# Performance work log

Hardware: AMD Instinct MI355X
Metric: run time of the kernel (lower is better)

## Reference

```python
import jax, jax.numpy as jnp
import numpy as np
import math

B, S, HID = 16, 1024, 1024
H, D = 16, 64  # heads, head_dim
WINDOW = 512  # pos bias length = 2*WINDOW+1 = 1025


def setup_inputs() -> dict:
    key = jax.random.key(0)
    ks = jax.random.split(key, 12)
    xav = lambda k, shp: jax.random.uniform(k, shp, jnp.float32, -1.0, 1.0) * math.sqrt(6.0 / (shp[0] + shp[1]))
    return {
        "hidden_states": jax.random.normal(ks[0], (B, S, HID), jnp.float32),
        "Wq": xav(ks[1], (HID, HID)), "bq": jnp.zeros((HID,), jnp.float32),
        "Wk": xav(ks[2], (HID, HID)), "bk": jnp.zeros((HID,), jnp.float32),
        "Wv": xav(ks[3], (HID, HID)), "bv": jnp.zeros((HID,), jnp.float32),
        "Wo": xav(ks[4], (HID, HID)), "bo": jnp.zeros((HID,), jnp.float32),
        "W_pe": xav(ks[5], (HID, 1)), "b_pe": jnp.zeros((HID,), jnp.float32),
        "pos_bias": 0.02 * jax.random.normal(ks[6], (1, H, 1, 2 * WINDOW + 1), jnp.float32),
        "clip_info": 0,
    }


def reference(hidden_states, Wq, bq, Wk, bk, Wv, bv, Wo, bo, W_pe, b_pe, pos_bias, clip_info):
    b, s, hid = hidden_states.shape
    mid = s // 2
    # relative positions in [-1, 1), shape [s, 1]
    positions = ((jnp.arange(s) - mid).astype(jnp.float32) / (mid + 1e-6))[:, None]
    pos_emb = positions @ W_pe.T + b_pe  # [s, hid]
    hs = hidden_states + pos_emb

    def heads(x):
        return x.reshape(b, s, H, D).transpose(0, 2, 1, 3)  # [b, H, s, D]

    q = heads(hs @ Wq.T + bq)
    k = heads(hs @ Wk.T + bk)
    v = heads(hs @ Wv.T + bv)

    scores = jnp.einsum("bhqd,bhkd->bhqk", q, k) / math.sqrt(D)
    scores = scores + pos_bias[:, :, :, :s]  # broadcast learned window bias over batch and query
    probs = jax.nn.softmax(scores, axis=-1)  # dropout is identity in eval mode
    ctx = jnp.einsum("bhqk,bhkd->bhqd", probs, v)
    ctx = ctx.transpose(0, 2, 1, 3).reshape(b, s, hid)
    return ctx @ Wo.T + bo
```

## Files before the change

kernel.cpp:

```cpp
#include <hip/hip_runtime.h>
#include <hip/hip_bf16.h>
#include <stdint.h>

#define BATCH 16
#define SEQ   1024
#define HIDN  1024
#define NH    16
#define HD    64
#define PBSTRIDE 1025

#define TS  64
#define AST 76

#define KSCL 0.18033688f
#define L2E  1.44269504f
#define MSUB 11.54156032f

#if __has_builtin(__builtin_amdgcn_exp2f)
#define EXP2(x) __builtin_amdgcn_exp2f(x)
#else
#define EXP2(x) exp2f(x)
#endif

typedef __attribute__((ext_vector_type(8))) short short8;
typedef __attribute__((ext_vector_type(4))) short short4v;
typedef __attribute__((ext_vector_type(4))) float f32x4;

__device__ __forceinline__ float bf2f(short x) {
    unsigned int u = ((unsigned int)(unsigned short)x) << 16;
    union { unsigned int u; float f; } c; c.u = u; return c.f;
}
__device__ __forceinline__ short f2bf(float f) {
    union { float f; unsigned int u; } c; c.f = f;
    unsigned int r = c.u + 0x7FFFu + ((c.u >> 16) & 1u);
    return (short)(r >> 16);
}
__device__ __forceinline__ short f2bf_fast(float f) {
    __hip_bfloat16 h = __float2bfloat16(f);
    return *reinterpret_cast<short*>(&h);
}

typedef __attribute__((address_space(1))) void gvoid;
typedef __attribute__((address_space(3))) void svoid;
__device__ __forceinline__ void gload_lds16(const void* g, void* l) {
    __builtin_amdgcn_global_load_lds((gvoid*)g, (svoid*)l, 16, 0, 0);
}

__global__ void convw4_k(const float* __restrict__ s0, const float* __restrict__ s1,
                         const float* __restrict__ s2, const float* __restrict__ s3,
                         short* __restrict__ d0, short* __restrict__ d1,
                         short* __restrict__ d2, short* __restrict__ d3) {
    const float* src = (blockIdx.y == 0) ? s0 : (blockIdx.y == 1) ? s1 : (blockIdx.y == 2) ? s2 : s3;
    short* dst       = (blockIdx.y == 0) ? d0 : (blockIdx.y == 1) ? d1 : (blockIdx.y == 2) ? d2 : d3;
    const float scl  = (blockIdx.y == 1) ? KSCL : 1.0f;
    int i = (blockIdx.x * 256 + threadIdx.x) * 4;
    float4 f = *(const float4*)(src + i);
    short4v o;
    o[0] = f2bf(f.x * scl); o[1] = f2bf(f.y * scl); o[2] = f2bf(f.z * scl); o[3] = f2bf(f.w * scl);
    *(short4v*)(dst + i) = o;
}

__global__ void convb_k(const float* __restrict__ b0, const float* __restrict__ b1,
                        const float* __restrict__ b2, float* __restrict__ fb) {
    int i = blockIdx.x * 256 + threadIdx.x;
    const float* s = (i < 1024) ? b0 : (i < 2048) ? b1 : b2;
    float scl = (i >= 1024 && i < 2048) ? KSCL : 1.0f;
    fb[i] = s[i & 1023] * scl;
}

__global__ void posemb_k(const float* __restrict__ hid, const float* __restrict__ wpe,
                         const float* __restrict__ bpe, short* __restrict__ hs) {
    long long idx = (long long)blockIdx.x * blockDim.x + threadIdx.x;
    long long base = idx * 8;
    int c = (int)(base & (HIDN - 1));
    int s = (int)((base >> 10) & (SEQ - 1));
    float pos = (float)(s - 512) * (1.0f / 512.0f);
    float4 h0 = *(const float4*)(hid + base);
    float4 h1 = *(const float4*)(hid + base + 4);
    float4 w0 = *(const float4*)(wpe + c);
    float4 w1 = *(const float4*)(wpe + c + 4);
    float4 b0 = *(const float4*)(bpe + c);
    float4 b1 = *(const float4*)(bpe + c + 4);
    short8 ov;
    ov[0] = f2bf(h0.x + pos * w0.x + b0.x);
    ov[1] = f2bf(h0.y + pos * w0.y + b0.y);
    ov[2] = f2bf(h0.z + pos * w0.z + b0.z);
    ov[3] = f2bf(h0.w + pos * w0.w + b0.w);
    ov[4] = f2bf(h1.x + pos * w1.x + b1.x);
    ov[5] = f2bf(h1.y + pos * w1.y + b1.y);
    ov[6] = f2bf(h1.z + pos * w1.z + b1.z);
    ov[7] = f2bf(h1.w + pos * w1.w + b1.w);
    *(short8*)(hs + base) = ov;
}

__global__ __launch_bounds__(256) void gemm_qkv(const short* __restrict__ A,
                                                const short* __restrict__ W,
                                                const float* __restrict__ fb,
                                                short* __restrict__ q,
                                                short* __restrict__ k,
                                                short* __restrict__ vt) {
    __shared__ __align__(16) short Als[2][128 * 64];
    __shared__ __align__(16) short Bls[2][128 * 64];
    const int tid  = threadIdx.x;
    const int lane = tid & 63;
    const int w    = tid >> 6;
    const int wr   = w >> 1, wc = w & 1;
    const int d0   = blockIdx.x;
    const int xcd  = d0 & 7;
    const int idx  = d0 >> 3;
    const int tx   = idx >> 4;
    const int ty   = xcd * 16 + (idx & 15);
    const int tm   = ty * 128;
    const int tn   = tx * 128;

    f32x4 acc[4][4] = {};

    const int srow = w * 32 + (lane >> 3);
    const int scol = ((lane & 7) ^ (lane >> 3)) * 8;
    const long long a_base = (long long)(tm + srow) * 1024 + scol;
    const long long b_base = (long long)(tn + srow) * 1024 + scol;
    const int ldsw = w * 4096;

    const int fr  = lane & 15;
    const int fg8 = (lane >> 4) * 8;
    const int frx = (lane & 7) * 8;

#pragma unroll
    for (int c = 0; c < 4; ++c) {
        gload_lds16((const void*)(A + a_base + (long long)c * 8 * 1024), (char*)Als[0] + ldsw + c * 1024);
        gload_lds16((const void*)(W + b_base + (long long)c * 8 * 1024), (char*)Bls[0] + ldsw + c * 1024);
    }
    asm volatile("s_waitcnt vmcnt(0)" ::: "memory");
    __syncthreads();

    int cur = 0;
    for (int k0 = 0; k0 < 1024; k0 += 64) {
        if (k0 + 64 < 1024) {
            const int nb = cur ^ 1;
#pragma unroll
            for (int c = 0; c < 4; ++c) {
                gload_lds16((const void*)(A + a_base + (long long)c * 8 * 1024 + k0 + 64),
                            (char*)Als[nb] + ldsw + c * 1024);
                gload_lds16((const void*)(W + b_base + (long long)c * 8 * 1024 + k0 + 64),
                            (char*)Bls[nb] + ldsw + c * 1024);
            }
        }
#pragma unroll
        for (int ks = 0; ks < 2; ++ks) {
            short8 af[4], bfr[4];
#pragma unroll
            for (int r = 0; r < 4; ++r) {
                af[r]  = *(const short8*)(Als[cur] + (wr * 64 + r * 16 + fr) * 64 + ((ks * 32 + fg8) ^ frx));
                bfr[r] = *(const short8*)(Bls[cur] + (wc * 64 + r * 16 + fr) * 64 + ((ks * 32 + fg8) ^ frx));
            }
#pragma unroll
            for (int mi = 0; mi < 4; ++mi)
#pragma unroll
                for (int ni = 0; ni < 4; ++ni)
                    acc[mi][ni] = __builtin_amdgcn_mfma_f32_16x16x32_bf16(af[mi], bfr[ni], acc[mi][ni], 0, 0, 0);
        }
        __syncthreads();
        cur ^= 1;
    }

    const int which = tn >> 10;
    const int g4 = (lane >> 4) * 4;
    if (which < 2) {
        short* dst = (which == 0) ? q : k;
#pragma unroll
        for (int ni = 0; ni < 4; ++ni) {
            int col = tn + wc * 64 + ni * 16 + fr;
            int cc  = col & 1023;
            int h   = cc >> 6, d = cc & 63;
            float bv = fb[col];
#pragma unroll
            for (int mi = 0; mi < 4; ++mi) {
#pragma unroll
                for (int r = 0; r < 4; ++r) {
                    int row = tm + wr * 64 + mi * 16 + g4 + r;
                    int b = row >> 10, s = row & 1023;
                    dst[(((long long)(b * NH + h) * SEQ + s) << 6) + d] = f2bf(acc[mi][ni][r] + bv);
                }
            }
        }
    } else {
#pragma unroll
        for (int ni = 0; ni < 4; ++ni) {
            int col = tn + wc * 64 + ni * 16 + fr;
            int cc  = col & 1023;
            int h   = cc >> 6, d = cc & 63;
            float bv = fb[col];
#pragma unroll
            for (int mi = 0; mi < 4; ++mi) {
                int row0 = tm + wr * 64 + mi * 16 + g4;
                int b = row0 >> 10, s0 = row0 & 1023;
                short4v o4;
#pragma unroll
                for (int r = 0; r < 4; ++r) o4[r] = f2bf(acc[mi][ni][r] + bv);
                *(short4v*)(vt + ((long long)(b * NH + h) * HD + d) * SEQ + s0) = o4;
            }
        }
    }
}

__global__ __launch_bounds__(256) void gemm_out(const short* __restrict__ A,
                                                const short* __restrict__ W,
                                                const float* __restrict__ bias,
                                                float* __restrict__ Cout) {
    __shared__ __align__(16) short Als[2][128 * 64];
    __shared__ __align__(16) short Bls[2][128 * 64];
    const int tid  = threadIdx.x;
    const int lane = tid & 63;
    const int w    = tid >> 6;
    const int wr   = w >> 1, wc = w & 1;
    const int d0   = blockIdx.x;
    const int xcd  = d0 & 7;
    const int idx  = d0 >> 3;
    const int tx   = idx >> 4;
    const int ty   = xcd * 16 + (idx & 15);
    const int tm   = ty * 128;
    const int tn   = tx * 128;

    f32x4 acc[4][4] = {};

    const int srow = w * 32 + (lane >> 3);
    const int scol = ((lane & 7) ^ (lane >> 3)) * 8;
    const long long a_base = (long long)(tm + srow) * 1024 + scol;
    const long long b_base = (long long)(tn + srow) * 1024 + scol;
    const int ldsw = w * 4096;

    const int fr  = lane & 15;
    const int fg8 = (lane >> 4) * 8;
    const int frx = (lane & 7) * 8;

#pragma unroll
    for (int c = 0; c < 4; ++c) {
        gload_lds16((const void*)(A + a_base + (long long)c * 8 * 1024), (char*)Als[0] + ldsw + c * 1024);
        gload_lds16((const void*)(W + b_base + (long long)c * 8 * 1024), (char*)Bls[0] + ldsw + c * 1024);
    }
    asm volatile("s_waitcnt vmcnt(0)" ::: "memory");
    __syncthreads();

    int cur = 0;
    for (int k0 = 0; k0 < 1024; k0 += 64) {
        if (k0 + 64 < 1024) {
            const int nb = cur ^ 1;
#pragma unroll
            for (int c = 0; c < 4; ++c) {
                gload_lds16((const void*)(A + a_base + (long long)c * 8 * 1024 + k0 + 64),
                            (char*)Als[nb] + ldsw + c * 1024);
                gload_lds16((const void*)(W + b_base + (long long)c * 8 * 1024 + k0 + 64),
                            (char*)Bls[nb] + ldsw + c * 1024);
            }
        }
#pragma unroll
        for (int ks = 0; ks < 2; ++ks) {
            short8 af[4], bfr[4];
#pragma unroll
            for (int r = 0; r < 4; ++r) {
                af[r]  = *(const short8*)(Als[cur] + (wr * 64 + r * 16 + fr) * 64 + ((ks * 32 + fg8) ^ frx));
                bfr[r] = *(const short8*)(Bls[cur] + (wc * 64 + r * 16 + fr) * 64 + ((ks * 32 + fg8) ^ frx));
            }
#pragma unroll
            for (int mi = 0; mi < 4; ++mi)
#pragma unroll
                for (int ni = 0; ni < 4; ++ni)
                    acc[mi][ni] = __builtin_amdgcn_mfma_f32_16x16x32_bf16(af[mi], bfr[ni], acc[mi][ni], 0, 0, 0);
        }
        __syncthreads();
        cur ^= 1;
    }

    const int g4 = (lane >> 4) * 4;
#pragma unroll
    for (int ni = 0; ni < 4; ++ni) {
        int col = tn + wc * 64 + ni * 16 + fr;
        float bv = bias[col];
#pragma unroll
        for (int mi = 0; mi < 4; ++mi)
#pragma unroll
            for (int r = 0; r < 4; ++r) {
                int row = tm + wr * 64 + mi * 16 + g4 + r;
                Cout[(long long)row * 1024 + col] = acc[mi][ni][r] + bv;
            }
    }
}

__global__ __launch_bounds__(256) void attn_k(const short* __restrict__ Q,
                                              const short* __restrict__ Kg,
                                              const short* __restrict__ Vt,
                                              const float* __restrict__ pbias,
                                              short* __restrict__ ctx) {
    __shared__ __align__(16) short Kls[2][64 * TS];
    __shared__ __align__(16) short Vls[2][64 * TS];
    __shared__ __align__(16) short Pls[4 * 32 * AST];

    const int tid  = threadIdx.x;
    const int lane = tid & 63;
    const int w    = tid >> 6;
    const int d0   = blockIdx.x;
    const int bh   = (d0 & 7) * 32 + (d0 >> 6);
    const int qt   = (d0 >> 3) & 7;
    const int h    = bh & (NH - 1);
    const long long base = (long long)bh * (SEQ * HD);

    const int fr = lane & 15;
    const int fg = lane >> 4;

    const int trow = w * 16 + (lane >> 3);
    const int scol = ((lane & 7) ^ (lane >> 3)) * 8;
    const int ldso = w * 1024;
    const long long kg0 = base + (long long)trow * HD + scol;
    const long long vg0 = base + (long long)trow * SEQ + scol;

    short8 qf[2][2];
#pragma unroll
    for (int mi = 0; mi < 2; ++mi)
#pragma unroll
        for (int ks = 0; ks < 2; ++ks)
            qf[mi][ks] = *(const short8*)(Q + base + (long long)(qt * 128 + w * 32 + mi * 16 + fr) * HD + ks * 32 + fg * 8);

    f32x4 o[2][4] = {};
    f32x4 osum[2] = {};
    short8 vones;
#pragma unroll
    for (int j = 0; j < 8; ++j) vones[j] = (short)0x3F80;

    short* Pw = Pls + w * 32 * AST;
    const float* pbh = pbias + h * PBSTRIDE;
    const int swc = (fr & 7) << 3;

    {
        const short* ks0 = Kg + kg0;
        const short* vs0 = Vt + vg0;
        gload_lds16(ks0,           Kls[0] + ldso);
        gload_lds16(ks0 + 8 * HD,  Kls[0] + ldso + 512);
        gload_lds16(vs0,           Vls[0] + ldso);
        gload_lds16(vs0 + 8 * SEQ, Vls[0] + ldso + 512);
    }
    float pbm[4];
#pragma unroll
    for (int ni = 0; ni < 4; ++ni)
        pbm[ni] = fmaf(pbh[ni * 16 + fr], L2E, -MSUB);
    asm volatile("s_waitcnt vmcnt(0)" ::: "memory");
    __syncthreads();

    int cur = 0;
    for (int kt = 0; kt < 16; ++kt) {
        if (kt < 15) {
            const int nb = cur ^ 1;
            const short* ks0 = Kg + kg0 + (long long)((kt + 1) * 64) * HD;
            const short* vs0 = Vt + vg0 + (kt + 1) * 64;
            gload_lds16(ks0,           Kls[nb] + ldso);
            gload_lds16(ks0 + 8 * HD,  Kls[nb] + ldso + 512);
            gload_lds16(vs0,           Vls[nb] + ldso);
            gload_lds16(vs0 + 8 * SEQ, Vls[nb] + ldso + 512);
        }

        f32x4 sc[2][4];
#pragma unroll
        for (int mi = 0; mi < 2; ++mi)
#pragma unroll
            for (int ni = 0; ni < 4; ++ni)
                sc[mi][ni] = (f32x4){pbm[ni], pbm[ni], pbm[ni], pbm[ni]};
        __builtin_amdgcn_s_setprio(1);
#pragma unroll
        for (int ks = 0; ks < 2; ++ks) {
#pragma unroll
            for (int ni = 0; ni < 4; ++ni) {
                short8 kb = *(const short8*)(Kls[cur] + (ni * 16 + fr) * TS + ((ks * 32 + fg * 8) ^ swc));
#pragma unroll
                for (int mi = 0; mi < 2; ++mi)
                    sc[mi][ni] = __builtin_amdgcn_mfma_f32_16x16x32_bf16(qf[mi][ks], kb, sc[mi][ni], 0, 0, 0);
            }
        }
        __builtin_amdgcn_s_setprio(0);

#pragma unroll
        for (int mi = 0; mi < 2; ++mi)
#pragma unroll
            for (int ni = 0; ni < 4; ++ni)
#pragma unroll
                for (int r = 0; r < 4; ++r)
                    Pw[(mi * 16 + fg * 4 + r) * AST + ni * 16 + fr] =
                        f2bf_fast(EXP2(sc[mi][ni][r]));

        {
            const int nkt = (kt + 1) & 15;
#pragma unroll
            for (int ni = 0; ni < 4; ++ni)
                pbm[ni] = fmaf(pbh[nkt * 64 + ni * 16 + fr], L2E, -MSUB);
        }

        __builtin_amdgcn_s_setprio(1);
#pragma unroll
        for (int ks = 0; ks < 2; ++ks) {
            short8 pa[2];
#pragma unroll
            for (int mi = 0; mi < 2; ++mi)
                pa[mi] = *(const short8*)(Pw + (mi * 16 + fr) * AST + ks * 32 + fg * 8);
            osum[0] = __builtin_amdgcn_mfma_f32_16x16x32_bf16(pa[0], vones, osum[0], 0, 0, 0);
            osum[1] = __builtin_amdgcn_mfma_f32_16x16x32_bf16(pa[1], vones, osum[1], 0, 0, 0);
#pragma unroll
            for (int di = 0; di < 4; ++di) {
                short8 vb = *(const short8*)(Vls[cur] + (di * 16 + fr) * TS + ((ks * 32 + fg * 8) ^ swc));
#pragma unroll
                for (int mi = 0; mi < 2; ++mi)
                    o[mi][di] = __builtin_amdgcn_mfma_f32_16x16x32_bf16(pa[mi], vb, o[mi][di], 0, 0, 0);
            }
        }
        __builtin_amdgcn_s_setprio(0);

        asm volatile("s_waitcnt vmcnt(0)" ::: "memory");
        __syncthreads();
        cur ^= 1;
    }

    const int b = bh >> 4;
#pragma unroll
    for (int mi = 0; mi < 2; ++mi) {
#pragma unroll
        for (int r = 0; r < 4; ++r) {
            float inv = 1.0f / osum[mi][r];
            int srow = qt * 128 + w * 32 + mi * 16 + fg * 4 + r;
#pragma unroll
            for (int di = 0; di < 4; ++di) {
                int d = di * 16 + fr;
                ctx[(long long)(b * SEQ + srow) * HIDN + h * HD + d] = f2bf(o[mi][di][r] * inv);
            }
        }
    }
}

extern "C" void kernel_launch(void* const* d_in, const int* in_sizes, int n_in,
                              void* d_out, int out_size, void* d_ws, size_t ws_size,
                              hipStream_t stream) {
    const float* hid  = (const float*)d_in[0];
    const float* Wq   = (const float*)d_in[1];
    const float* bq   = (const float*)d_in[2];
    const float* Wk   = (const float*)d_in[3];
    const float* bk   = (const float*)d_in[4];
    const float* Wv   = (const float*)d_in[5];
    const float* bv   = (const float*)d_in[6];
    const float* Wo   = (const float*)d_in[7];
    const float* bo   = (const float*)d_in[8];
    const float* Wpe  = (const float*)d_in[9];
    const float* bpe  = (const float*)d_in[10];
    const float* pbias = (const float*)d_in[11];

    const long long NE = (long long)BATCH * SEQ * HIDN;
    const long long WSZ = (long long)HIDN * HIDN;

    short* hs   = (short*)d_ws;
    short* vt   = hs + NE;
    short* Wcq  = vt + NE;
    short* Wck  = Wcq + WSZ;
    short* Wcv  = Wck + WSZ;
    short* Wco  = Wcv + WSZ;
    float* fb   = (float*)(Wco + WSZ);
    short* q    = (short*)d_out;
    short* k    = q + NE;
    short* ctx  = hs;

    posemb_k<<<(int)(NE / 8 / 256), 256, 0, stream>>>(hid, Wpe, bpe, hs);
    convw4_k<<<dim3((int)(WSZ / 4 / 256), 4), 256, 0, stream>>>(Wq, Wk, Wv, Wo, Wcq, Wck, Wcv, Wco);
    convb_k<<<12, 256, 0, stream>>>(bq, bk, bv, fb);

    gemm_qkv<<<3072, 256, 0, stream>>>(hs, Wcq, fb, q, k, vt);

    attn_k<<<2048, 256, 0, stream>>>(q, k, vt, pbias, ctx);

    gemm_out<<<1024, 256, 0, stream>>>(ctx, Wco, bo, (float*)d_out);
}
```

Before: 338.2 us.

## Enlarge attention blocks to 256 query rows with 8 waves and truncate P to bf16

The attention kernel now uses 512-thread blocks that each cover 256 query rows, which halves the grid. Each K/V tile loaded into LDS is shared by twice as many waves, and every thread issues half as many global-to-LDS loads. The block-to-(batch-head, query-tile) mapping is adjusted to keep the XCD grouping. Separately, the probability conversion to bf16 now truncates instead of rounding, which saves ALU work but adds a small bias in precision. The P scratch buffer in LDS doubles, which may reduce how many blocks can be resident at once.

```diff
diff --git a/kernel.cpp b/kernel.cpp
--- a/kernel.cpp
+++ b/kernel.cpp
@@ -35,9 +35,9 @@
     unsigned int r = c.u + 0x7FFFu + ((c.u >> 16) & 1u);
     return (short)(r >> 16);
 }
-__device__ __forceinline__ short f2bf_fast(float f) {
-    __hip_bfloat16 h = __float2bfloat16(f);
-    return *reinterpret_cast<short*>(&h);
+__device__ __forceinline__ short f2bf_trunc(float f) {
+    union { float f; unsigned int u; } c; c.f = f;
+    return (short)(c.u >> 16);
 }
 
 typedef __attribute__((address_space(1))) void gvoid;
@@ -286,30 +286,32 @@
     }
 }
 
-__global__ __launch_bounds__(256) void attn_k(const short* __restrict__ Q,
+__global__ __launch_bounds__(512) void attn_k(const short* __restrict__ Q,
                                               const short* __restrict__ Kg,
                                               const short* __restrict__ Vt,
                                               const float* __restrict__ pbias,
                                               short* __restrict__ ctx) {
     __shared__ __align__(16) short Kls[2][64 * TS];
     __shared__ __align__(16) short Vls[2][64 * TS];
-    __shared__ __align__(16) short Pls[4 * 32 * AST];
+    __shared__ __align__(16) short Pls[8 * 32 * AST];
 
     const int tid  = threadIdx.x;
     const int lane = tid & 63;
     const int w    = tid >> 6;
     const int d0   = blockIdx.x;
-    const int bh   = (d0 & 7) * 32 + (d0 >> 6);
-    const int qt   = (d0 >> 3) & 7;
+    const int xcd  = d0 & 7;
+    const int idx  = d0 >> 3;
+    const int bh   = xcd * 32 + (idx >> 2);
+    const int qt   = idx & 3;
     const int h    = bh & (NH - 1);
     const long long base = (long long)bh * (SEQ * HD);
 
     const int fr = lane & 15;
     const int fg = lane >> 4;
 
-    const int trow = w * 16 + (lane >> 3);
+    const int trow = w * 8 + (lane >> 3);
     const int scol = ((lane & 7) ^ (lane >> 3)) * 8;
-    const int ldso = w * 1024;
+    const int ldso = w * 512;
     const long long kg0 = base + (long long)trow * HD + scol;
     const long long vg0 = base + (long long)trow * SEQ + scol;
 
@@ -318,7 +320,7 @@
     for (int mi = 0; mi < 2; ++mi)
 #pragma unroll
         for (int ks = 0; ks < 2; ++ks)
-            qf[mi][ks] = *(const short8*)(Q + base + (long long)(qt * 128 + w * 32 + mi * 16 + fr) * HD + ks * 32 + fg * 8);
+            qf[mi][ks] = *(const short8*)(Q + base + (long long)(qt * 256 + w * 32 + mi * 16 + fr) * HD + ks * 32 + fg * 8);
 
     f32x4 o[2][4] = {};
     f32x4 osum[2] = {};
@@ -330,14 +332,8 @@
     const float* pbh = pbias + h * PBSTRIDE;
     const int swc = (fr & 7) << 3;
 
-    {
-        const short* ks0 = Kg + kg0;
-        const short* vs0 = Vt + vg0;
-        gload_lds16(ks0,           Kls[0] + ldso);
-        gload_lds16(ks0 + 8 * HD,  Kls[0] + ldso + 512);
-        gload_lds16(vs0,           Vls[0] + ldso);
-        gload_lds16(vs0 + 8 * SEQ, Vls[0] + ldso + 512);
-    }
+    gload_lds16(Kg + kg0, Kls[0] + ldso);
+    gload_lds16(Vt + vg0, Vls[0] + ldso);
     float pbm[4];
 #pragma unroll
     for (int ni = 0; ni < 4; ++ni)
@@ -349,12 +345,8 @@
     for (int kt = 0; kt < 16; ++kt) {
         if (kt < 15) {
             const int nb = cur ^ 1;
-            const short* ks0 = Kg + kg0 + (long long)((kt + 1) * 64) * HD;
-            const short* vs0 = Vt + vg0 + (kt + 1) * 64;
-            gload_lds16(ks0,           Kls[nb] + ldso);
-            gload_lds16(ks0 + 8 * HD,  Kls[nb] + ldso + 512);
-            gload_lds16(vs0,           Vls[nb] + ldso);
-            gload_lds16(vs0 + 8 * SEQ, Vls[nb] + ldso + 512);
+            gload_lds16(Kg + kg0 + (long long)((kt + 1) * 64) * HD, Kls[nb] + ldso);
+            gload_lds16(Vt + vg0 + (kt + 1) * 64,                   Vls[nb] + ldso);
         }
 
         f32x4 sc[2][4];
@@ -383,7 +375,7 @@
 #pragma unroll
                 for (int r = 0; r < 4; ++r)
                     Pw[(mi * 16 + fg * 4 + r) * AST + ni * 16 + fr] =
-                        f2bf_fast(EXP2(sc[mi][ni][r]));
+                        f2bf_trunc(EXP2(sc[mi][ni][r]));
 
         {
             const int nkt = (kt + 1) & 15;
@@ -422,7 +414,7 @@
 #pragma unroll
         for (int r = 0; r < 4; ++r) {
             float inv = 1.0f / osum[mi][r];
-            int srow = qt * 128 + w * 32 + mi * 16 + fg * 4 + r;
+            int srow = qt * 256 + w * 32 + mi * 16 + fg * 4 + r;
 #pragma unroll
             for (int di = 0; di < 4; ++di) {
                 int d = di * 16 + fr;
@@ -468,7 +460,7 @@
 
     gemm_qkv<<<3072, 256, 0, stream>>>(hs, Wcq, fb, q, k, vt);
 
-    attn_k<<<2048, 256, 0, stream>>>(q, k, vt, pbias, ctx);
+    attn_k<<<1024, 512, 0, stream>>>(q, k, vt, pbias, ctx);
 
     gemm_out<<<1024, 256, 0, stream>>>(ctx, Wco, bo, (float*)d_out);
 }
```

Measured after the change: 324.6 us. -4.0%, faster.
